# Optimization experiments

Measured on AMD Instinct MI355X. Metric: run time of the kernel, lower is better.

The kernel has to match this reference:

```python
import math
import jax, jax.numpy as jnp
import numpy as np

B, LA, LB, H = 32, 1024, 1024, 1024


def setup_inputs() -> dict:
    key = jax.random.key(0)
    k1, k2, k3, k4 = jax.random.split(key, 4)
    a = jax.random.normal(k1, (B, LA, H), dtype=jnp.float32)
    b = jax.random.normal(k2, (B, LB, H), dtype=jnp.float32)
    mask_a = jax.random.randint(k3, (B, LA, 1), 0, 2, dtype=jnp.int32)
    mask_b = jax.random.randint(k4, (B, LB, 1), 0, 2, dtype=jnp.int32)
    temperature = jnp.asarray(1.0 / math.sqrt(H), dtype=jnp.float32)
    return {"a": a, "b": b, "mask_a": mask_a, "mask_b": mask_b,
            "temperature": temperature}


def reference(a, b, mask_a, mask_b, temperature):
    # attn: [B, La, Lb] scaled cross-attention scores
    attn = jnp.einsum("bsh,bth->bst", a, b) * temperature
    # outer product of per-token validity -> pairwise valid mask [B, La, Lb]
    mask = jnp.einsum("bsi,bti->bst",
                      mask_a.astype(jnp.float32),
                      mask_b.astype(jnp.float32)).astype(bool)
    attn = jnp.where(mask, attn, jnp.float32(-10000.0))
    attn_a = jax.nn.softmax(attn, axis=1)  # normalize over La
    attn_b = jax.nn.softmax(attn, axis=2)  # normalize over Lb
    feature_b = jnp.einsum("bst,bsh->bth", attn_a, a)  # [B, Lb, H]
    feature_a = jnp.einsum("bst,bth->bsh", attn_b, b)  # [B, La, H]
    return feature_a, feature_b
```

## Files before the change

### kernel.cpp

```cpp
#include <hip/hip_runtime.h>

#define NB 32
#define L 1024
#define H 1024

typedef __attribute__((ext_vector_type(4))) float floatx4;
typedef __attribute__((ext_vector_type(8))) short shortx8;
typedef __attribute__((ext_vector_type(8))) unsigned short ushortx8;

__device__ __forceinline__ unsigned short f2bf(float f) {
    union { float f; unsigned int u; } v; v.f = f;
    unsigned int u = v.u;
    u += 0x7fffu + ((u >> 16) & 1u);
    return (unsigned short)(u >> 16);
}
__device__ __forceinline__ float bf2f(unsigned short h) {
    union { unsigned int u; float f; } v; v.u = ((unsigned int)h) << 16;
    return v.f;
}

__device__ __forceinline__ void gload_lds16(const void* g, void* l) {
    __builtin_amdgcn_global_load_lds(
        (const __attribute__((address_space(1))) unsigned int*)g,
        (__attribute__((address_space(3))) unsigned int*)l, 16, 0, 0);
}

__device__ __forceinline__ void swz_tile(int nb, int& bi_l, int& tx, int& ty) {
    int fid = blockIdx.x;
    int wid = (fid & 7) * (nb * 8) + (fid >> 3);
    bi_l = wid >> 6;
    int t = wid & 63;
    tx = t & 7;
    ty = t >> 3;
}

__global__ void detect_kernel(const unsigned short* a, int* flag) {
    int tid = threadIdx.x;
    unsigned short u = a[tid];
    int e = (u >> 7) & 0xff;
    int ok = (u == 0) || (e >= 116 && e <= 136);
    unsigned long long ball = __ballot(ok != 0);
    if (tid == 0) flag[0] = (__popcll(ball) >= 56) ? 1 : 0;
}

__device__ __forceinline__ void store_out(void* out, size_t eidx, float v, int isbf) {
    if (isbf) ((unsigned short*)out)[eidx] = f2bf(v);
    else      ((float*)out)[eidx] = v;
}

__global__ __launch_bounds__(256) void convT_kernel(
    const void* A, const void* Bm, const int* flag,
    unsigned short* a_c, unsigned short* b_c,
    unsigned short* aT, unsigned short* bT,
    float* mean_a, float* mean_b, int b0) {
    __shared__ __align__(16) unsigned short T[64][80];
    int z = blockIdx.z;
    int which = z & 1, bi_l = z >> 1, bi = b0 + bi_l;
    int s0 = blockIdx.y * 64, h0 = blockIdx.x * 64;
    const void* src = which ? Bm : A;
    unsigned short* xc = which ? b_c : a_c;
    unsigned short* xT = which ? bT : aT;
    float* msum = which ? mean_b : mean_a;
    int isbf = flag[0];
    int tid = threadIdx.x;

    int r = tid >> 2, c0 = (tid & 3) * 16;
    size_t gin = (size_t)bi * L * H + (size_t)(s0 + r) * H + h0 + c0;
    unsigned short v[16];
    if (isbf) {
        const unsigned short* p = (const unsigned short*)src + gin;
        *(ushortx8*)&v[0] = *(const ushortx8*)p;
        *(ushortx8*)&v[8] = *(const ushortx8*)(p + 8);
    } else {
        const float* p = (const float*)src + gin;
#pragma unroll
        for (int u = 0; u < 16; u += 4) {
            float4 f = *(const float4*)(p + u);
            v[u] = f2bf(f.x); v[u + 1] = f2bf(f.y);
            v[u + 2] = f2bf(f.z); v[u + 3] = f2bf(f.w);
        }
    }
    *(ushortx8*)&T[r][c0] = *(const ushortx8*)&v[0];
    *(ushortx8*)&T[r][c0 + 8] = *(const ushortx8*)&v[8];
    if (!isbf) {
        size_t gco = (size_t)bi_l * L * H + (size_t)(s0 + r) * H + h0 + c0;
        *(ushortx8*)&xc[gco] = *(const ushortx8*)&v[0];
        *(ushortx8*)&xc[gco + 8] = *(const ushortx8*)&v[8];
    }
    __syncthreads();

    int hr = tid >> 2, sc0 = (tid & 3) * 16;
    unsigned short tv2[16];
    float ms = 0.f;
#pragma unroll
    for (int u = 0; u < 16; ++u) {
        unsigned short q = T[sc0 + u][hr];
        tv2[u] = q;
        ms += bf2f(q);
    }
    size_t gto = (size_t)bi_l * (size_t)H * L + (size_t)(h0 + hr) * L + s0 + sc0;
    *(ushortx8*)&xT[gto] = *(const ushortx8*)&tv2[0];
    *(ushortx8*)&xT[gto + 8] = *(const ushortx8*)&tv2[8];
    ms += __shfl_xor(ms, 1);
    ms += __shfl_xor(ms, 2);
    if ((tid & 3) == 0) atomicAdd(&msum[bi * H + h0 + hr], ms);
}

__global__ __launch_bounds__(256) void wtrans_kernel(const unsigned short* w,
                                                     unsigned short* wT) {
    __shared__ __align__(16) unsigned short T[64][80];
    int bi_l = blockIdx.z;
    int s0 = blockIdx.y * 64, t0 = blockIdx.x * 64;
    int tid = threadIdx.x;
    int r = tid >> 2, c0 = (tid & 3) * 16;
    size_t gin = (size_t)bi_l * L * L + (size_t)(s0 + r) * L + t0 + c0;
    *(ushortx8*)&T[r][c0] = *(const ushortx8*)&w[gin];
    *(ushortx8*)&T[r][c0 + 8] = *(const ushortx8*)&w[gin + 8];
    __syncthreads();
    int tr = tid >> 2, sc0 = (tid & 3) * 16;
    unsigned short o[16];
#pragma unroll
    for (int u = 0; u < 16; ++u) o[u] = T[sc0 + u][tr];
    size_t gout = (size_t)bi_l * L * L + (size_t)(t0 + tr) * L + s0 + sc0;
    *(ushortx8*)&wT[gout] = *(const ushortx8*)&o[0];
    *(ushortx8*)&wT[gout + 8] = *(const ushortx8*)&o[8];
}

__device__ __forceinline__ void stage_tiles(
    const unsigned short* Arow, const unsigned short* Brow,
    int lda, int ldb, int k0,
    unsigned short* As, unsigned short* Bs, int tid) {
#pragma unroll
    for (int it = 0; it < 4; ++it) {
        int idx = (it & 1) * 256 + tid;
        int rr = idx >> 2, cc = (idx & 3) * 8;
        const unsigned short* src = (it < 2)
            ? (Arow + (size_t)rr * lda + k0 + cc)
            : (Brow + (size_t)rr * ldb + k0 + cc);
        unsigned short* dst = ((it < 2) ? As : Bs) + idx * 8;
        gload_lds16(src, dst);
    }
}

__device__ __forceinline__ void gemm_kk_pipe(
    const unsigned short* Arow, const unsigned short* Brow,
    int lda, int ldb, int K,
    unsigned short* lds,
    int tid, floatx4 (&acc)[4][4]) {
    int lane = tid & 63, wid = tid >> 6;
    int wm = wid >> 1, wn = wid & 1;
    int lane15 = lane & 15, quad = lane >> 4;
    unsigned short* As0 = lds;
    unsigned short* Bs0 = lds + 4096;
    unsigned short* As1 = lds + 8192;
    unsigned short* Bs1 = lds + 12288;
    int NT = K >> 5;

    stage_tiles(Arow, Brow, lda, ldb, 0, As0, Bs0, tid);
    stage_tiles(Arow, Brow, lda, ldb, 32, As1, Bs1, tid);

    for (int t = 0; t < NT; ++t) {
        unsigned short* As = (t & 1) ? As1 : As0;
        unsigned short* Bs = (t & 1) ? Bs1 : Bs0;
        if (t < NT - 1) asm volatile("s_waitcnt vmcnt(4)" ::: "memory");
        else            asm volatile("s_waitcnt vmcnt(0)" ::: "memory");
        __builtin_amdgcn_s_barrier();
        asm volatile("" ::: "memory");
        shortx8 af[4], bfr[4];
#pragma unroll
        for (int i = 0; i < 4; ++i)
            af[i] = *(const shortx8*)(As + (wm * 64 + i * 16 + lane15) * 32 + quad * 8);
#pragma unroll
        for (int j = 0; j < 4; ++j)
            bfr[j] = *(const shortx8*)(Bs + (wn * 64 + j * 16 + lane15) * 32 + quad * 8);
        asm volatile("s_waitcnt lgkmcnt(0)" ::: "memory");
        __builtin_amdgcn_sched_barrier(0);
        __builtin_amdgcn_s_barrier();
        asm volatile("" ::: "memory");
        if (t + 2 < NT)
            stage_tiles(Arow, Brow, lda, ldb, (t + 2) * 32, As, Bs, tid);
        __builtin_amdgcn_s_setprio(1);
#pragma unroll
        for (int i = 0; i < 4; ++i)
#pragma unroll
            for (int j = 0; j < 4; ++j)
                acc[i][j] = __builtin_amdgcn_mfma_f32_16x16x32_bf16(af[i], bfr[j], acc[i][j], 0, 0, 0);
        __builtin_amdgcn_s_setprio(0);
    }
    __builtin_amdgcn_s_barrier();
}

__global__ __launch_bounds__(256) void score_kernel(
    const void* Araw, const void* Braw,
    const unsigned short* a_c, const unsigned short* b_c,
    const int* mask_a, const int* mask_b, const void* temp, const int* flag,
    unsigned short* w, float* row_l, float* col_l, int b0, int nb) {
    __shared__ __align__(16) unsigned short lds[16384];
    int bi_l, tx, ty;
    swz_tile(nb, bi_l, tx, ty);
    int bi = b0 + bi_l;
    int s0 = ty * 128, t0 = tx * 128;
    int tid = threadIdx.x;
    int isbf = flag[0];

    floatx4 acc[4][4];
#pragma unroll
    for (int i = 0; i < 4; ++i)
#pragma unroll
        for (int j = 0; j < 4; ++j)
#pragma unroll
            for (int rr = 0; rr < 4; ++rr) acc[i][j][rr] = 0.f;

    const unsigned short* Arow = isbf
        ? (const unsigned short*)Araw + (size_t)bi * L * H + (size_t)s0 * H
        : a_c + (size_t)bi_l * L * H + (size_t)s0 * H;
    const unsigned short* Brow = isbf
        ? (const unsigned short*)Braw + (size_t)bi * L * H + (size_t)t0 * H
        : b_c + (size_t)bi_l * L * H + (size_t)t0 * H;
    gemm_kk_pipe(Arow, Brow, H, H, H, lds, tid, acc);

    float tv = isbf ? bf2f(((const unsigned short*)temp)[0]) : ((const float*)temp)[0];
    int lane = tid & 63, wid = tid >> 6;
    int wm = wid >> 1, wn = wid & 1;
    int lane15 = lane & 15, quad = lane >> 4;

    int mb[4];
#pragma unroll
    for (int j = 0; j < 4; ++j)
        mb[j] = mask_b[bi * L + t0 + wn * 64 + j * 16 + lane15];
    size_t wbase = (size_t)bi_l * L * L;
    float colp[4] = {0.f, 0.f, 0.f, 0.f};
#pragma unroll
    for (int i = 0; i < 4; ++i) {
#pragma unroll
        for (int r = 0; r < 4; ++r) {
            int s = s0 + wm * 64 + i * 16 + quad * 4 + r;
            int ma = mask_a[bi * L + s];
            float rp = 0.f;
#pragma unroll
            for (int j = 0; j < 4; ++j) {
                int t = t0 + wn * 64 + j * 16 + lane15;
                float wv = (ma && mb[j]) ? __expf(acc[i][j][r] * tv) : 0.f;
                unsigned short wq = f2bf(wv);
                w[wbase + (size_t)s * L + t] = wq;
                float wf = bf2f(wq);
                rp += wf;
                colp[j] += wf;
            }
            rp += __shfl_xor(rp, 1);
            rp += __shfl_xor(rp, 2);
            rp += __shfl_xor(rp, 4);
            rp += __shfl_xor(rp, 8);
            if (lane15 == 0) atomicAdd(&row_l[bi * L + s], rp);
        }
    }
#pragma unroll
    for (int j = 0; j < 4; ++j) {
        float cp = colp[j];
        cp += __shfl_xor(cp, 16);
        cp += __shfl_xor(cp, 32);
        if (quad == 0) {
            int t = t0 + wn * 64 + j * 16 + lane15;
            atomicAdd(&col_l[bi * L + t], cp);
        }
    }
}

__global__ __launch_bounds__(256) void feat_a_kernel(
    const unsigned short* w, const unsigned short* bT, const int* mask_a,
    const int* flag, const float* row_l, const float* mean_b, void* out,
    int b0, int nb) {
    __shared__ __align__(16) unsigned short lds[16384];
    int bi_l, tx, ty;
    swz_tile(nb, bi_l, tx, ty);
    int bi = b0 + bi_l;
    int s0 = ty * 128, h0 = tx * 128;
    int tid = threadIdx.x;

    floatx4 acc[4][4];
#pragma unroll
    for (int i = 0; i < 4; ++i)
#pragma unroll
        for (int j = 0; j < 4; ++j)
#pragma unroll
            for (int rr = 0; rr < 4; ++rr) acc[i][j][rr] = 0.f;

    gemm_kk_pipe(w + (size_t)bi_l * L * L + (size_t)s0 * L,
                 bT + (size_t)bi_l * (size_t)H * L + (size_t)h0 * L,
                 L, L, L, lds, tid, acc);

    int isbf = flag[0];
    int lane = tid & 63, wid = tid >> 6;
    int wm = wid >> 1, wn = wid & 1;
    int lane15 = lane & 15, quad = lane >> 4;
    const float invL = 1.f / (float)L;
#pragma unroll
    for (int i = 0; i < 4; ++i) {
#pragma unroll
        for (int r = 0; r < 4; ++r) {
            int s = s0 + wm * 64 + i * 16 + quad * 4 + r;
            int ma = mask_a[bi * L + s];
            float scale = ma ? (1.f / row_l[bi * L + s]) : 0.f;
#pragma unroll
            for (int j = 0; j < 4; ++j) {
                int h = h0 + wn * 64 + j * 16 + lane15;
                float v = ma ? acc[i][j][r] * scale : mean_b[bi * H + h] * invL;
                store_out(out, (size_t)bi * L * H + (size_t)s * H + h, v, isbf);
            }
        }
    }
}

__global__ __launch_bounds__(256) void feat_b_kernel(
    const unsigned short* wT, const unsigned short* aT, const int* mask_b,
    const int* flag, const float* col_l, const float* mean_a, void* out,
    int b0, int nb) {
    __shared__ __align__(16) unsigned short lds[16384];
    int bi_l, tx, ty;
    swz_tile(nb, bi_l, tx, ty);
    int bi = b0 + bi_l;
    int t0 = ty * 128, h0 = tx * 128;
    int tid = threadIdx.x;

    floatx4 acc[4][4];
#pragma unroll
    for (int i = 0; i < 4; ++i)
#pragma unroll
        for (int j = 0; j < 4; ++j)
#pragma unroll
            for (int rr = 0; rr < 4; ++rr) acc[i][j][rr] = 0.f;

    gemm_kk_pipe(wT + (size_t)bi_l * L * L + (size_t)t0 * L,
                 aT + (size_t)bi_l * (size_t)H * L + (size_t)h0 * L,
                 L, L, L, lds, tid, acc);

    int isbf = flag[0];
    int lane = tid & 63, wid = tid >> 6;
    int wm = wid >> 1, wn = wid & 1;
    int lane15 = lane & 15, quad = lane >> 4;
    const float invL = 1.f / (float)L;
    const size_t FEAT_B_OFF = (size_t)NB * L * H;
#pragma unroll
    for (int i = 0; i < 4; ++i) {
#pragma unroll
        for (int r = 0; r < 4; ++r) {
            int t = t0 + wm * 64 + i * 16 + quad * 4 + r;
            int mbv = mask_b[bi * L + t];
            float scale = mbv ? (1.f / col_l[bi * L + t]) : 0.f;
#pragma unroll
            for (int j = 0; j < 4; ++j) {
                int h = h0 + wn * 64 + j * 16 + lane15;
                float v = mbv ? acc[i][j][r] * scale : mean_a[bi * H + h] * invL;
                store_out(out, FEAT_B_OFF + (size_t)bi * L * H + (size_t)t * H + h, v, isbf);
            }
        }
    }
}

extern "C" void kernel_launch(void* const* d_in, const int* in_sizes, int n_in,
                              void* d_out, int out_size, void* d_ws, size_t ws_size,
                              hipStream_t stream) {
    const void* a = d_in[0];
    const void* b = d_in[1];
    const int* mask_a = (const int*)d_in[2];
    const int* mask_b = (const int*)d_in[3];
    const void* temp = d_in[4];

    char* wsp = (char*)d_ws;
    float* row_l  = (float*)wsp;
    float* col_l  = row_l + (size_t)NB * L;
    float* mean_a = col_l + (size_t)NB * L;
    float* mean_b = mean_a + (size_t)NB * H;
    int*   flag   = (int*)(mean_b + (size_t)NB * H);
    const size_t stats_bytes = ((size_t)NB * L * 2 + (size_t)NB * H * 2) * 4 + 256;

    const size_t per_batch = 6 * (size_t)L * H * 2;
    size_t wavail = (ws_size > stats_bytes) ? ws_size - stats_bytes : 0;
    int chunk = (int)(wavail / per_batch);
    if (chunk < 1) chunk = 1;
    if (chunk > NB) chunk = NB;

    unsigned short* a_c  = (unsigned short*)(wsp + stats_bytes);
    unsigned short* b_c  = a_c + (size_t)chunk * L * H;
    unsigned short* aT   = b_c + (size_t)chunk * L * H;
    unsigned short* bT   = aT  + (size_t)chunk * L * H;
    unsigned short* wbuf = bT  + (size_t)chunk * L * H;
    unsigned short* wT   = wbuf + (size_t)chunk * L * L;

    hipMemsetAsync(d_ws, 0, stats_bytes, stream);
    detect_kernel<<<1, 64, 0, stream>>>((const unsigned short*)a, flag);

    for (int b0 = 0; b0 < NB; b0 += chunk) {
        int nb = (NB - b0 < chunk) ? (NB - b0) : chunk;
        convT_kernel<<<dim3(16, 16, nb * 2), 256, 0, stream>>>(
            a, b, flag, a_c, b_c, aT, bT, mean_a, mean_b, b0);
        score_kernel<<<dim3(nb * 64), 256, 0, stream>>>(
            a, b, a_c, b_c, mask_a, mask_b, temp, flag, wbuf,
            row_l, col_l, b0, nb);
        wtrans_kernel<<<dim3(16, 16, nb), 256, 0, stream>>>(wbuf, wT);
        feat_a_kernel<<<dim3(nb * 64), 256, 0, stream>>>(
            wbuf, bT, mask_a, flag, row_l, mean_b, d_out, b0, nb);
        feat_b_kernel<<<dim3(nb * 64), 256, 0, stream>>>(
            wT, aT, mask_b, flag, col_l, mean_a, d_out, b0, nb);
    }
}
```

Measured before the change: 889.4 us.

## Triple-buffer GEMM LDS pipeline and XOR-swizzle LDS layout to avoid bank conflicts

The shared GEMM mainloop goes from double to triple buffering, prefetching three K-tiles ahead with adjusted vmcnt waits, to hide more global-load latency. The LDS tile layout is XOR-swizzled on the 16-byte column groups, and the read side is updated to match, to reduce LDS bank conflicts on the MFMA fragment loads. LDS per block grows from 32KB to 48KB, which may lower occupancy. K is now hardcoded to 1024 (NT=32).

```diff
diff --git a/kernel.cpp b/kernel.cpp
--- a/kernel.cpp
+++ b/kernel.cpp
@@ -133,10 +133,11 @@
 #pragma unroll
     for (int it = 0; it < 4; ++it) {
         int idx = (it & 1) * 256 + tid;
-        int rr = idx >> 2, cc = (idx & 3) * 8;
+        int rr = idx >> 2;
+        int gs = (idx & 3) ^ ((rr >> 1) & 3);
         const unsigned short* src = (it < 2)
-            ? (Arow + (size_t)rr * lda + k0 + cc)
-            : (Brow + (size_t)rr * ldb + k0 + cc);
+            ? (Arow + (size_t)rr * lda + k0 + gs * 8)
+            : (Brow + (size_t)rr * ldb + k0 + gs * 8);
         unsigned short* dst = ((it < 2) ? As : Bs) + idx * 8;
         gload_lds16(src, dst);
     }
@@ -144,41 +145,41 @@
 
 __device__ __forceinline__ void gemm_kk_pipe(
     const unsigned short* Arow, const unsigned short* Brow,
-    int lda, int ldb, int K,
+    int lda, int ldb,
     unsigned short* lds,
     int tid, floatx4 (&acc)[4][4]) {
+    const int NT = 32;
     int lane = tid & 63, wid = tid >> 6;
     int wm = wid >> 1, wn = wid & 1;
     int lane15 = lane & 15, quad = lane >> 4;
-    unsigned short* As0 = lds;
-    unsigned short* Bs0 = lds + 4096;
-    unsigned short* As1 = lds + 8192;
-    unsigned short* Bs1 = lds + 12288;
-    int NT = K >> 5;
-
-    stage_tiles(Arow, Brow, lda, ldb, 0, As0, Bs0, tid);
-    stage_tiles(Arow, Brow, lda, ldb, 32, As1, Bs1, tid);
-
+    int gsw = (quad ^ ((lane15 >> 1) & 3)) * 8;
+
+    stage_tiles(Arow, Brow, lda, ldb, 0,  lds,         lds + 4096,  tid);
+    stage_tiles(Arow, Brow, lda, ldb, 32, lds + 8192,  lds + 12288, tid);
+    stage_tiles(Arow, Brow, lda, ldb, 64, lds + 16384, lds + 20480, tid);
+
+    int p = 0;
     for (int t = 0; t < NT; ++t) {
-        unsigned short* As = (t & 1) ? As1 : As0;
-        unsigned short* Bs = (t & 1) ? Bs1 : Bs0;
-        if (t < NT - 1) asm volatile("s_waitcnt vmcnt(4)" ::: "memory");
-        else            asm volatile("s_waitcnt vmcnt(0)" ::: "memory");
+        unsigned short* As = lds + p * 8192;
+        unsigned short* Bs = As + 4096;
+        if (t < NT - 2)      asm volatile("s_waitcnt vmcnt(8)" ::: "memory");
+        else if (t == NT - 2) asm volatile("s_waitcnt vmcnt(4)" ::: "memory");
+        else                 asm volatile("s_waitcnt vmcnt(0)" ::: "memory");
         __builtin_amdgcn_s_barrier();
         asm volatile("" ::: "memory");
         shortx8 af[4], bfr[4];
 #pragma unroll
         for (int i = 0; i < 4; ++i)
-            af[i] = *(const shortx8*)(As + (wm * 64 + i * 16 + lane15) * 32 + quad * 8);
+            af[i] = *(const shortx8*)(As + (wm * 64 + i * 16 + lane15) * 32 + gsw);
 #pragma unroll
         for (int j = 0; j < 4; ++j)
-            bfr[j] = *(const shortx8*)(Bs + (wn * 64 + j * 16 + lane15) * 32 + quad * 8);
+            bfr[j] = *(const shortx8*)(Bs + (wn * 64 + j * 16 + lane15) * 32 + gsw);
         asm volatile("s_waitcnt lgkmcnt(0)" ::: "memory");
         __builtin_amdgcn_sched_barrier(0);
         __builtin_amdgcn_s_barrier();
         asm volatile("" ::: "memory");
-        if (t + 2 < NT)
-            stage_tiles(Arow, Brow, lda, ldb, (t + 2) * 32, As, Bs, tid);
+        if (t + 3 < NT)
+            stage_tiles(Arow, Brow, lda, ldb, (t + 3) * 32, As, Bs, tid);
         __builtin_amdgcn_s_setprio(1);
 #pragma unroll
         for (int i = 0; i < 4; ++i)
@@ -186,6 +187,7 @@
             for (int j = 0; j < 4; ++j)
                 acc[i][j] = __builtin_amdgcn_mfma_f32_16x16x32_bf16(af[i], bfr[j], acc[i][j], 0, 0, 0);
         __builtin_amdgcn_s_setprio(0);
+        p = (p == 2) ? 0 : p + 1;
     }
     __builtin_amdgcn_s_barrier();
 }
@@ -195,7 +197,7 @@
     const unsigned short* a_c, const unsigned short* b_c,
     const int* mask_a, const int* mask_b, const void* temp, const int* flag,
     unsigned short* w, float* row_l, float* col_l, int b0, int nb) {
-    __shared__ __align__(16) unsigned short lds[16384];
+    __shared__ __align__(16) unsigned short lds[24576];
     int bi_l, tx, ty;
     swz_tile(nb, bi_l, tx, ty);
     int bi = b0 + bi_l;
@@ -217,7 +219,7 @@
     const unsigned short* Brow = isbf
         ? (const unsigned short*)Braw + (size_t)bi * L * H + (size_t)t0 * H
         : b_c + (size_t)bi_l * L * H + (size_t)t0 * H;
-    gemm_kk_pipe(Arow, Brow, H, H, H, lds, tid, acc);
+    gemm_kk_pipe(Arow, Brow, H, H, lds, tid, acc);
 
     float tv = isbf ? bf2f(((const unsigned short*)temp)[0]) : ((const float*)temp)[0];
     int lane = tid & 63, wid = tid >> 6;
@@ -270,7 +272,7 @@
     const unsigned short* w, const unsigned short* bT, const int* mask_a,
     const int* flag, const float* row_l, const float* mean_b, void* out,
     int b0, int nb) {
-    __shared__ __align__(16) unsigned short lds[16384];
+    __shared__ __align__(16) unsigned short lds[24576];
     int bi_l, tx, ty;
     swz_tile(nb, bi_l, tx, ty);
     int bi = b0 + bi_l;
@@ -287,7 +289,7 @@
 
     gemm_kk_pipe(w + (size_t)bi_l * L * L + (size_t)s0 * L,
                  bT + (size_t)bi_l * (size_t)H * L + (size_t)h0 * L,
-                 L, L, L, lds, tid, acc);
+                 L, L, lds, tid, acc);
 
     int isbf = flag[0];
     int lane = tid & 63, wid = tid >> 6;
@@ -315,7 +317,7 @@
     const unsigned short* wT, const unsigned short* aT, const int* mask_b,
     const int* flag, const float* col_l, const float* mean_a, void* out,
     int b0, int nb) {
-    __shared__ __align__(16) unsigned short lds[16384];
+    __shared__ __align__(16) unsigned short lds[24576];
     int bi_l, tx, ty;
     swz_tile(nb, bi_l, tx, ty);
     int bi = b0 + bi_l;
@@ -332,7 +334,7 @@
 
     gemm_kk_pipe(wT + (size_t)bi_l * L * L + (size_t)t0 * L,
                  aT + (size_t)bi_l * (size_t)H * L + (size_t)h0 * L,
-                 L, L, L, lds, tid, acc);
+                 L, L, lds, tid, acc);
 
     int isbf = flag[0];
     int lane = tid & 63, wid = tid >> 6;
```

Result: no change. 872.1 us (-1.9%).

## Enlarge GEMM tiles to 256x256 with 512 threads and XOR-swizzled LDS

Applied to the files above, without the earlier changes.

Replaces the 128x128 tile, 256-thread GEMM core used by the score and feature kernels with a 256x256 tile computed by 512 threads (8 waves) over K-steps of 64. The LDS staging uses an XOR swizzle to avoid bank conflicts, and double buffering is restructured to prefetch the next tile while computing on the current one. The grid swizzle and launch shapes change to match. The aim is higher arithmetic intensity and fewer global reloads per output, at the cost of 128 KB of LDS per block and many more accumulator registers. That register and LDS load may limit occupancy or cause spills, and the 128 KB LDS per block may not allow the requested two blocks per CU.

```diff
diff --git a/kernel.cpp b/kernel.cpp
--- a/kernel.cpp
+++ b/kernel.cpp
@@ -25,13 +25,13 @@
         (__attribute__((address_space(3))) unsigned int*)l, 16, 0, 0);
 }
 
-__device__ __forceinline__ void swz_tile(int nb, int& bi_l, int& tx, int& ty) {
+__device__ __forceinline__ void swz256(int nb, int& bi_l, int& tx, int& ty) {
     int fid = blockIdx.x;
-    int wid = (fid & 7) * (nb * 8) + (fid >> 3);
-    bi_l = wid >> 6;
-    int t = wid & 63;
-    tx = t & 7;
-    ty = t >> 3;
+    int wid = (fid & 7) * (nb * 2) + (fid >> 3);
+    bi_l = wid >> 4;
+    int t = wid & 15;
+    tx = t & 3;
+    ty = t >> 2;
 }
 
 __global__ void detect_kernel(const unsigned short* a, int* flag) {
@@ -126,90 +126,97 @@
     *(ushortx8*)&wT[gout + 8] = *(const ushortx8*)&o[8];
 }
 
-__device__ __forceinline__ void stage_tiles(
+__device__ __forceinline__ void stage256(
+    const unsigned short* Arow, const unsigned short* Brow, int k0,
+    unsigned short* As, unsigned short* Bs, int tid) {
+#pragma unroll
+    for (int l = 0; l < 4; ++l) {
+        int idx = l * 512 + tid;
+        int row = idx >> 3;
+        int g = (idx & 7) ^ (row & 7);
+        gload_lds16(Arow + (size_t)row * 1024 + k0 + g * 8, As + idx * 8);
+    }
+#pragma unroll
+    for (int l = 0; l < 4; ++l) {
+        int idx = l * 512 + tid;
+        int row = idx >> 3;
+        int g = (idx & 7) ^ (row & 7);
+        gload_lds16(Brow + (size_t)row * 1024 + k0 + g * 8, Bs + idx * 8);
+    }
+}
+
+__device__ __forceinline__ void gemm256_pipe(
     const unsigned short* Arow, const unsigned short* Brow,
-    int lda, int ldb, int k0,
-    unsigned short* As, unsigned short* Bs, int tid) {
-#pragma unroll
-    for (int it = 0; it < 4; ++it) {
-        int idx = (it & 1) * 256 + tid;
-        int rr = idx >> 2, cc = (idx & 3) * 8;
-        const unsigned short* src = (it < 2)
-            ? (Arow + (size_t)rr * lda + k0 + cc)
-            : (Brow + (size_t)rr * ldb + k0 + cc);
-        unsigned short* dst = ((it < 2) ? As : Bs) + idx * 8;
-        gload_lds16(src, dst);
-    }
-}
-
-__device__ __forceinline__ void gemm_kk_pipe(
-    const unsigned short* Arow, const unsigned short* Brow,
-    int lda, int ldb, int K,
     unsigned short* lds,
-    int tid, floatx4 (&acc)[4][4]) {
+    int tid, floatx4 (&acc)[8][4]) {
+    const int NT = 16;
     int lane = tid & 63, wid = tid >> 6;
-    int wm = wid >> 1, wn = wid & 1;
+    int wm = wid >> 2, wn = wid & 3;
     int lane15 = lane & 15, quad = lane >> 4;
-    unsigned short* As0 = lds;
-    unsigned short* Bs0 = lds + 4096;
-    unsigned short* As1 = lds + 8192;
-    unsigned short* Bs1 = lds + 12288;
-    int NT = K >> 5;
-
-    stage_tiles(Arow, Brow, lda, ldb, 0, As0, Bs0, tid);
-    stage_tiles(Arow, Brow, lda, ldb, 32, As1, Bs1, tid);
+    int l7 = lane15 & 7;
+
+    stage256(Arow, Brow, 0, lds, lds + 16384, tid);
+    asm volatile("s_waitcnt vmcnt(0)" ::: "memory");
+    __builtin_amdgcn_s_barrier();
+    asm volatile("" ::: "memory");
 
     for (int t = 0; t < NT; ++t) {
-        unsigned short* As = (t & 1) ? As1 : As0;
-        unsigned short* Bs = (t & 1) ? Bs1 : Bs0;
-        if (t < NT - 1) asm volatile("s_waitcnt vmcnt(4)" ::: "memory");
-        else            asm volatile("s_waitcnt vmcnt(0)" ::: "memory");
+        unsigned short* cur = lds + (t & 1) * 32768;
+        unsigned short* nxt = lds + ((t & 1) ^ 1) * 32768;
+        if (t + 1 < NT)
+            stage256(Arow, Brow, (t + 1) * 64, nxt, nxt + 16384, tid);
+#pragma unroll
+        for (int ks = 0; ks < 2; ++ks) {
+            shortx8 af[8], bf[4];
+#pragma unroll
+            for (int m = 0; m < 8; ++m) {
+                int row = wm * 128 + m * 16 + lane15;
+                int col = (ks * 4 + quad) ^ l7;
+                af[m] = *(const shortx8*)(cur + row * 64 + col * 8);
+            }
+#pragma unroll
+            for (int n = 0; n < 4; ++n) {
+                int row = wn * 64 + n * 16 + lane15;
+                int col = (ks * 4 + quad) ^ l7;
+                bf[n] = *(const shortx8*)(cur + 16384 + row * 64 + col * 8);
+            }
+            asm volatile("s_waitcnt lgkmcnt(0)" ::: "memory");
+            __builtin_amdgcn_sched_barrier(0);
+            __builtin_amdgcn_s_setprio(1);
+#pragma unroll
+            for (int m = 0; m < 8; ++m)
+#pragma unroll
+                for (int n = 0; n < 4; ++n)
+                    acc[m][n] = __builtin_amdgcn_mfma_f32_16x16x32_bf16(
+                        af[m], bf[n], acc[m][n], 0, 0, 0);
+            __builtin_amdgcn_s_setprio(0);
+        }
+        asm volatile("s_waitcnt vmcnt(0)" ::: "memory");
         __builtin_amdgcn_s_barrier();
         asm volatile("" ::: "memory");
-        shortx8 af[4], bfr[4];
-#pragma unroll
-        for (int i = 0; i < 4; ++i)
-            af[i] = *(const shortx8*)(As + (wm * 64 + i * 16 + lane15) * 32 + quad * 8);
-#pragma unroll
-        for (int j = 0; j < 4; ++j)
-            bfr[j] = *(const shortx8*)(Bs + (wn * 64 + j * 16 + lane15) * 32 + quad * 8);
-        asm volatile("s_waitcnt lgkmcnt(0)" ::: "memory");
-        __builtin_amdgcn_sched_barrier(0);
-        __builtin_amdgcn_s_barrier();
-        asm volatile("" ::: "memory");
-        if (t + 2 < NT)
-            stage_tiles(Arow, Brow, lda, ldb, (t + 2) * 32, As, Bs, tid);
-        __builtin_amdgcn_s_setprio(1);
-#pragma unroll
-        for (int i = 0; i < 4; ++i)
-#pragma unroll
-            for (int j = 0; j < 4; ++j)
-                acc[i][j] = __builtin_amdgcn_mfma_f32_16x16x32_bf16(af[i], bfr[j], acc[i][j], 0, 0, 0);
-        __builtin_amdgcn_s_setprio(0);
-    }
-    __builtin_amdgcn_s_barrier();
-}
-
-__global__ __launch_bounds__(256) void score_kernel(
+    }
+}
+
+__global__ __launch_bounds__(512, 2) void score_kernel(
     const void* Araw, const void* Braw,
     const unsigned short* a_c, const unsigned short* b_c,
     const int* mask_a, const int* mask_b, const void* temp, const int* flag,
     unsigned short* w, float* row_l, float* col_l, int b0, int nb) {
-    __shared__ __align__(16) unsigned short lds[16384];
+    __shared__ __align__(16) unsigned short lds[65536];
     int bi_l, tx, ty;
-    swz_tile(nb, bi_l, tx, ty);
+    swz256(nb, bi_l, tx, ty);
     int bi = b0 + bi_l;
-    int s0 = ty * 128, t0 = tx * 128;
+    int s0 = ty * 256, t0 = tx * 256;
     int tid = threadIdx.x;
     int isbf = flag[0];
 
-    floatx4 acc[4][4];
-#pragma unroll
-    for (int i = 0; i < 4; ++i)
-#pragma unroll
-        for (int j = 0; j < 4; ++j)
-#pragma unroll
-            for (int rr = 0; rr < 4; ++rr) acc[i][j][rr] = 0.f;
+    floatx4 acc[8][4];
+#pragma unroll
+    for (int m = 0; m < 8; ++m)
+#pragma unroll
+        for (int n = 0; n < 4; ++n)
+#pragma unroll
+            for (int rr = 0; rr < 4; ++rr) acc[m][n][rr] = 0.f;
 
     const unsigned short* Arow = isbf
         ? (const unsigned short*)Araw + (size_t)bi * L * H + (size_t)s0 * H
@@ -217,35 +224,35 @@
     const unsigned short* Brow = isbf
         ? (const unsigned short*)Braw + (size_t)bi * L * H + (size_t)t0 * H
         : b_c + (size_t)bi_l * L * H + (size_t)t0 * H;
-    gemm_kk_pipe(Arow, Brow, H, H, H, lds, tid, acc);
+    gemm256_pipe(Arow, Brow, lds, tid, acc);
 
     float tv = isbf ? bf2f(((const unsigned short*)temp)[0]) : ((const float*)temp)[0];
     int lane = tid & 63, wid = tid >> 6;
-    int wm = wid >> 1, wn = wid & 1;
+    int wm = wid >> 2, wn = wid & 3;
     int lane15 = lane & 15, quad = lane >> 4;
 
-    int mb[4];
-#pragma unroll
-    for (int j = 0; j < 4; ++j)
-        mb[j] = mask_b[bi * L + t0 + wn * 64 + j * 16 + lane15];
+    int mbv[4];
+#pragma unroll
+    for (int n = 0; n < 4; ++n)
+        mbv[n] = mask_b[bi * L + t0 + wn * 64 + n * 16 + lane15];
     size_t wbase = (size_t)bi_l * L * L;
     float colp[4] = {0.f, 0.f, 0.f, 0.f};
 #pragma unroll
-    for (int i = 0; i < 4; ++i) {
+    for (int m = 0; m < 8; ++m) {
 #pragma unroll
         for (int r = 0; r < 4; ++r) {
-            int s = s0 + wm * 64 + i * 16 + quad * 4 + r;
+            int s = s0 + wm * 128 + m * 16 + quad * 4 + r;
             int ma = mask_a[bi * L + s];
             float rp = 0.f;
 #pragma unroll
-            for (int j = 0; j < 4; ++j) {
-                int t = t0 + wn * 64 + j * 16 + lane15;
-                float wv = (ma && mb[j]) ? __expf(acc[i][j][r] * tv) : 0.f;
+            for (int n = 0; n < 4; ++n) {
+                int t = t0 + wn * 64 + n * 16 + lane15;
+                float wv = (ma && mbv[n]) ? __expf(acc[m][n][r] * tv) : 0.f;
                 unsigned short wq = f2bf(wv);
                 w[wbase + (size_t)s * L + t] = wq;
                 float wf = bf2f(wq);
                 rp += wf;
-                colp[j] += wf;
+                colp[n] += wf;
             }
             rp += __shfl_xor(rp, 1);
             rp += __shfl_xor(rp, 2);
@@ -255,102 +262,102 @@
         }
     }
 #pragma unroll
-    for (int j = 0; j < 4; ++j) {
-        float cp = colp[j];
+    for (int n = 0; n < 4; ++n) {
+        float cp = colp[n];
         cp += __shfl_xor(cp, 16);
         cp += __shfl_xor(cp, 32);
         if (quad == 0) {
-            int t = t0 + wn * 64 + j * 16 + lane15;
+            int t = t0 + wn * 64 + n * 16 + lane15;
             atomicAdd(&col_l[bi * L + t], cp);
         }
     }
 }
 
-__global__ __launch_bounds__(256) void feat_a_kernel(
+__global__ __launch_bounds__(512, 2) void feat_a_kernel(
     const unsigned short* w, const unsigned short* bT, const int* mask_a,
     const int* flag, const float* row_l, const float* mean_b, void* out,
     int b0, int nb) {
-    __shared__ __align__(16) unsigned short lds[16384];
+    __shared__ __align__(16) unsigned short lds[65536];
     int bi_l, tx, ty;
-    swz_tile(nb, bi_l, tx, ty);
+    swz256(nb, bi_l, tx, ty);
     int bi = b0 + bi_l;
-    int s0 = ty * 128, h0 = tx * 128;
-    int tid = threadIdx.x;
-
-    floatx4 acc[4][4];
-#pragma unroll
-    for (int i = 0; i < 4; ++i)
-#pragma unroll
-        for (int j = 0; j < 4; ++j)
-#pragma unroll
-            for (int rr = 0; rr < 4; ++rr) acc[i][j][rr] = 0.f;
-
-    gemm_kk_pipe(w + (size_t)bi_l * L * L + (size_t)s0 * L,
+    int s0 = ty * 256, h0 = tx * 256;
+    int tid = threadIdx.x;
+
+    floatx4 acc[8][4];
+#pragma unroll
+    for (int m = 0; m < 8; ++m)
+#pragma unroll
+        for (int n = 0; n < 4; ++n)
+#pragma unroll
+            for (int rr = 0; rr < 4; ++rr) acc[m][n][rr] = 0.f;
+
+    gemm256_pipe(w + (size_t)bi_l * L * L + (size_t)s0 * L,
                  bT + (size_t)bi_l * (size_t)H * L + (size_t)h0 * L,
-                 L, L, L, lds, tid, acc);
+                 lds, tid, acc);
 
     int isbf = flag[0];
     int lane = tid & 63, wid = tid >> 6;
-    int wm = wid >> 1, wn = wid & 1;
+    int wm = wid >> 2, wn = wid & 3;
     int lane15 = lane & 15, quad = lane >> 4;
     const float invL = 1.f / (float)L;
 #pragma unroll
-    for (int i = 0; i < 4; ++i) {
+    for (int m = 0; m < 8; ++m) {
 #pragma unroll
         for (int r = 0; r < 4; ++r) {
-            int s = s0 + wm * 64 + i * 16 + quad * 4 + r;
+            int s = s0 + wm * 128 + m * 16 + quad * 4 + r;
             int ma = mask_a[bi * L + s];
             float scale = ma ? (1.f / row_l[bi * L + s]) : 0.f;
 #pragma unroll
-            for (int j = 0; j < 4; ++j) {
-                int h = h0 + wn * 64 + j * 16 + lane15;
-                float v = ma ? acc[i][j][r] * scale : mean_b[bi * H + h] * invL;
+            for (int n = 0; n < 4; ++n) {
+                int h = h0 + wn * 64 + n * 16 + lane15;
+                float v = ma ? acc[m][n][r] * scale : mean_b[bi * H + h] * invL;
                 store_out(out, (size_t)bi * L * H + (size_t)s * H + h, v, isbf);
             }
         }
     }
 }
 
-__global__ __launch_bounds__(256) void feat_b_kernel(
+__global__ __launch_bounds__(512, 2) void feat_b_kernel(
     const unsigned short* wT, const unsigned short* aT, const int* mask_b,
     const int* flag, const float* col_l, const float* mean_a, void* out,
     int b0, int nb) {
-    __shared__ __align__(16) unsigned short lds[16384];
+    __shared__ __align__(16) unsigned short lds[65536];
     int bi_l, tx, ty;
-    swz_tile(nb, bi_l, tx, ty);
+    swz256(nb, bi_l, tx, ty);
     int bi = b0 + bi_l;
-    int t0 = ty * 128, h0 = tx * 128;
-    int tid = threadIdx.x;
-
-    floatx4 acc[4][4];
-#pragma unroll
-    for (int i = 0; i < 4; ++i)
-#pragma unroll
-        for (int j = 0; j < 4; ++j)
-#pragma unroll
-            for (int rr = 0; rr < 4; ++rr) acc[i][j][rr] = 0.f;
-
-    gemm_kk_pipe(wT + (size_t)bi_l * L * L + (size_t)t0 * L,
+    int t0 = ty * 256, h0 = tx * 256;
+    int tid = threadIdx.x;
+
+    floatx4 acc[8][4];
+#pragma unroll
+    for (int m = 0; m < 8; ++m)
+#pragma unroll
+        for (int n = 0; n < 4; ++n)
+#pragma unroll
+            for (int rr = 0; rr < 4; ++rr) acc[m][n][rr] = 0.f;
+
+    gemm256_pipe(wT + (size_t)bi_l * L * L + (size_t)t0 * L,
                  aT + (size_t)bi_l * (size_t)H * L + (size_t)h0 * L,
-                 L, L, L, lds, tid, acc);
+                 lds, tid, acc);
 
     int isbf = flag[0];
     int lane = tid & 63, wid = tid >> 6;
-    int wm = wid >> 1, wn = wid & 1;
+    int wm = wid >> 2, wn = wid & 3;
     int lane15 = lane & 15, quad = lane >> 4;
     const float invL = 1.f / (float)L;
     const size_t FEAT_B_OFF = (size_t)NB * L * H;
 #pragma unroll
-    for (int i = 0; i < 4; ++i) {
+    for (int m = 0; m < 8; ++m) {
 #pragma unroll
         for (int r = 0; r < 4; ++r) {
-            int t = t0 + wm * 64 + i * 16 + quad * 4 + r;
-            int mbv = mask_b[bi * L + t];
-            float scale = mbv ? (1.f / col_l[bi * L + t]) : 0.f;
-#pragma unroll
-            for (int j = 0; j < 4; ++j) {
-                int h = h0 + wn * 64 + j * 16 + lane15;
-                float v = mbv ? acc[i][j][r] * scale : mean_a[bi * H + h] * invL;
+            int t = t0 + wm * 128 + m * 16 + quad * 4 + r;
+            int mv = mask_b[bi * L + t];
+            float scale = mv ? (1.f / col_l[bi * L + t]) : 0.f;
+#pragma unroll
+            for (int n = 0; n < 4; ++n) {
+                int h = h0 + wn * 64 + n * 16 + lane15;
+                float v = mv ? acc[m][n][r] * scale : mean_a[bi * H + h] * invL;
                 store_out(out, FEAT_B_OFF + (size_t)bi * L * H + (size_t)t * H + h, v, isbf);
             }
         }
@@ -394,13 +401,13 @@
         int nb = (NB - b0 < chunk) ? (NB - b0) : chunk;
         convT_kernel<<<dim3(16, 16, nb * 2), 256, 0, stream>>>(
             a, b, flag, a_c, b_c, aT, bT, mean_a, mean_b, b0);
-        score_kernel<<<dim3(nb * 64), 256, 0, stream>>>(
+        score_kernel<<<dim3(nb * 16), 512, 0, stream>>>(
             a, b, a_c, b_c, mask_a, mask_b, temp, flag, wbuf,
             row_l, col_l, b0, nb);
         wtrans_kernel<<<dim3(16, 16, nb), 256, 0, stream>>>(wbuf, wT);
-        feat_a_kernel<<<dim3(nb * 64), 256, 0, stream>>>(
+        feat_a_kernel<<<dim3(nb * 16), 512, 0, stream>>>(
             wbuf, bT, mask_a, flag, row_l, mean_b, d_out, b0, nb);
-        feat_b_kernel<<<dim3(nb * 64), 256, 0, stream>>>(
+        feat_b_kernel<<<dim3(nb * 16), 512, 0, stream>>>(
             wT, aT, mask_b, flag, col_l, mean_a, d_out, b0, nb);
     }
 }
```

Measured after the change: 820.5 us. 1.08x faster.
